# Kernel optimization log

Hardware: AMD Instinct MI355X
Metric: run time of the kernel (lower is better)

## Reference

```python
import jax, jax.numpy as jnp
import numpy as np

B, DIM, SIZE = 16, 512, 128

def _conv2d(x, w, pad_h, pad_w):
    # x: [B,C,H,W], w: [O,I,kh,kw]
    return jax.lax.conv_general_dilated(
        x, w, window_strides=(1, 1),
        padding=((pad_h, pad_h), (pad_w, pad_w)),
        dimension_numbers=('NCHW', 'OIHW', 'NCHW'))


def setup_inputs() -> dict:
    key = jax.random.key(0)
    ks = jax.random.split(key, 8)
    s = SIZE
    return {
        'x': jax.random.normal(ks[0], (B, DIM, s, s), dtype=jnp.float32),
        'w_conv': jax.random.normal(ks[1], (2, DIM, 1, 1), dtype=jnp.float32) * (1.0 / np.sqrt(DIM)),
        'w_ww_conv': jax.random.normal(ks[2], (1, 2, s, 5), dtype=jnp.float32) * (1.0 / np.sqrt(2 * s * 5)),
        'w_hw_conv': jax.random.normal(ks[3], (1, 2, 5, s), dtype=jnp.float32) * (1.0 / np.sqrt(2 * s * 5)),
        'ww_lin_w': jax.random.normal(ks[4], (s, s), dtype=jnp.float32) * (1.0 / np.sqrt(s)),
        'ww_lin_b': jax.random.normal(ks[5], (s,), dtype=jnp.float32) * 0.01,
        'hw_lin_w': jax.random.normal(ks[6], (s, s), dtype=jnp.float32) * (1.0 / np.sqrt(s)),
        'hw_lin_b': jax.random.normal(ks[7], (s,), dtype=jnp.float32) * 0.01,
    }


def reference(x, w_conv, w_ww_conv, w_hw_conv, ww_lin_w, ww_lin_b, hw_lin_w, hw_lin_b):
    # 1x1 conv dim -> 2 (no bias, no bn, no act): pure channel GEMM
    x2 = jnp.einsum('bchw,oc->bohw', x, w_conv[:, :, 0, 0])  # [B,2,S,S]

    # ww branch: conv kernel (SIZE,5), pad (0,2) -> [B,1,1,S]
    ww = _conv2d(x2, w_ww_conv, 0, 2)[:, 0, 0, :]            # [B,S]
    ww = jax.nn.sigmoid(ww @ ww_lin_w.T + ww_lin_b)          # Linear + Sigmoid

    # hw branch: conv kernel (5,SIZE), pad (2,0) -> [B,1,S,1]
    hw = _conv2d(x2, w_hw_conv, 2, 0)[:, 0, :, 0]            # [B,S]
    hw = jax.nn.sigmoid(hw @ hw_lin_w.T + hw_lin_b)

    # batched outer product hw (S,1) @ ww (1,S) -> [B,S,S]
    return jnp.einsum('bh,bw->bhw', hw, ww)
```

## Files before the change

kernel.cpp:

```cpp
#include <hip/hip_runtime.h>
#include <math.h>

#define BB   16
#define CC   512
#define SS   128
#define HWSZ (SS * SS)
#define NCH  16
#define CK   (CC / NCH)

__global__ __launch_bounds__(1024) void k1a_partial(
    const float* __restrict__ x, const float* __restrict__ wconv,
    float* __restrict__ part)
{
    const int b   = blockIdx.x >> 4;
    const int ck  = blockIdx.x & (NCH - 1);
    const int tid = threadIdx.x;

    const float* xp = x + ((size_t)b * CC + (size_t)ck * CK) * HWSZ + tid * 4;
    const float* wA = wconv + ck * CK;
    const float* wB = wconv + CC + ck * CK;

    float4 a0[4], a1[4];
    #pragma unroll
    for (int s = 0; s < 4; ++s) {
        a0[s] = make_float4(0.f, 0.f, 0.f, 0.f);
        a1[s] = make_float4(0.f, 0.f, 0.f, 0.f);
    }

    #pragma unroll 2
    for (int c = 0; c < CK; ++c) {
        const float wa = wA[c];
        const float wb = wB[c];
        #pragma unroll
        for (int s = 0; s < 4; ++s) {
            const float4 v = *(const float4*)(xp + (size_t)c * HWSZ + s * 4096);
            a0[s].x = fmaf(v.x, wa, a0[s].x);
            a0[s].y = fmaf(v.y, wa, a0[s].y);
            a0[s].z = fmaf(v.z, wa, a0[s].z);
            a0[s].w = fmaf(v.w, wa, a0[s].w);
            a1[s].x = fmaf(v.x, wb, a1[s].x);
            a1[s].y = fmaf(v.y, wb, a1[s].y);
            a1[s].z = fmaf(v.z, wb, a1[s].z);
            a1[s].w = fmaf(v.w, wb, a1[s].w);
        }
    }

    float* pp = part + (size_t)(b * NCH + ck) * 2 * HWSZ + tid * 4;
    #pragma unroll
    for (int s = 0; s < 4; ++s) {
        *(float4*)(pp + s * 4096)        = a0[s];
        *(float4*)(pp + HWSZ + s * 4096) = a1[s];
    }
}

__global__ __launch_bounds__(256) void k1b_reduce(
    const float* __restrict__ part, float* __restrict__ x2,
    float* __restrict__ x2t)
{
    const int pc  = blockIdx.x & 15;
    const int o   = (blockIdx.x >> 4) & 1;
    const int b   = blockIdx.x >> 5;
    const int tid = threadIdx.x;

    const int p = (pc * 256 + tid) * 4;

    const float* pp = part + ((size_t)(b * NCH) * 2 + o) * HWSZ + p;
    float4 s = make_float4(0.f, 0.f, 0.f, 0.f);
    #pragma unroll
    for (int ck = 0; ck < NCH; ++ck) {
        const float4 v = *(const float4*)(pp + (size_t)ck * 2 * HWSZ);
        s.x += v.x; s.y += v.y; s.z += v.z; s.w += v.w;
    }

    *(float4*)&x2[(size_t)(b * 2 + o) * HWSZ + p] = s;

    const int h  = p >> 7;
    const int w0 = p & 127;
    float* t = x2t + ((size_t)(b * 2 + o) * SS + w0) * SS + h;
    t[0 * SS] = s.x;
    t[1 * SS] = s.y;
    t[2 * SS] = s.z;
    t[3 * SS] = s.w;
}

__global__ __launch_bounds__(512) void k2_rest(
    const float* __restrict__ x2, const float* __restrict__ x2t,
    const float* __restrict__ wwc,
    const float* __restrict__ hwc,
    const float* __restrict__ wlw, const float* __restrict__ wlb,
    const float* __restrict__ hlw, const float* __restrict__ hlb,
    float* __restrict__ out)
{
    __shared__ float tw[2][5][SS];
    __shared__ float uh[2][5][SS];
    __shared__ float vbuf[2 * SS];
    __shared__ float rbuf[2 * SS];

    const int b        = blockIdx.x;
    const int tid      = threadIdx.x;
    const int lane_pos = tid & 127;
    const int q        = tid >> 7;
    const int half     = q & 1;
    const int half_u   = __builtin_amdgcn_readfirstlane(half);

    if (q < 2) {
        const float* xrow = x2 + (size_t)(b * 2 + half) * HWSZ + lane_pos;
        const float* wrow = wwc + half_u * (SS * 5);
        float acc[5] = {0.f, 0.f, 0.f, 0.f, 0.f};
        #pragma unroll 8
        for (int kh = 0; kh < SS; ++kh) {
            const float xv = xrow[(size_t)kh * SS];
            #pragma unroll
            for (int kw = 0; kw < 5; ++kw)
                acc[kw] = fmaf(xv, wrow[kh * 5 + kw], acc[kw]);
        }
        #pragma unroll
        for (int kw = 0; kw < 5; ++kw) tw[half][kw][lane_pos] = acc[kw];
    } else {
        const float* xcol = x2t + (size_t)(b * 2 + half) * HWSZ + lane_pos;
        const float* wrow = hwc + half_u * (5 * SS);
        float acc[5] = {0.f, 0.f, 0.f, 0.f, 0.f};
        #pragma unroll 8
        for (int kw = 0; kw < SS; ++kw) {
            const float xv = xcol[(size_t)kw * SS];
            #pragma unroll
            for (int kh = 0; kh < 5; ++kh)
                acc[kh] = fmaf(xv, wrow[kh * SS + kw], acc[kh]);
        }
        #pragma unroll
        for (int kh = 0; kh < 5; ++kh) uh[half][kh][lane_pos] = acc[kh];
    }
    __syncthreads();

    if (tid < 256) {
        float s = 0.f;
        if (half == 0) {
            const int wo = lane_pos;
            #pragma unroll
            for (int kw = 0; kw < 5; ++kw) {
                const int wsrc = wo + kw - 2;
                if (wsrc >= 0 && wsrc < SS) s += tw[0][kw][wsrc] + tw[1][kw][wsrc];
            }
        } else {
            const int ho = lane_pos;
            #pragma unroll
            for (int kh = 0; kh < 5; ++kh) {
                const int hsrc = ho + kh - 2;
                if (hsrc >= 0 && hsrc < SS) s += uh[0][kh][hsrc] + uh[1][kh][hsrc];
            }
        }
        vbuf[tid] = s;
    }
    __syncthreads();

    if (tid < 256) {
        const int j = lane_pos;
        const float* lw  = (half == 0) ? wlw : hlw;
        const float* lb  = (half == 0) ? wlb : hlb;
        const float* vin = vbuf + half * SS;
        float s = lb[j];
        const float4* wr = (const float4*)(lw + (size_t)j * SS);
        #pragma unroll 4
        for (int k4 = 0; k4 < SS / 4; ++k4) {
            const float4 wv = wr[k4];
            s = fmaf(vin[4 * k4 + 0], wv.x, s);
            s = fmaf(vin[4 * k4 + 1], wv.y, s);
            s = fmaf(vin[4 * k4 + 2], wv.z, s);
            s = fmaf(vin[4 * k4 + 3], wv.w, s);
        }
        rbuf[tid] = 1.f / (1.f + expf(-s));
    }
    __syncthreads();

    {
        float* ob = out + (size_t)b * HWSZ;
        for (int p4 = tid; p4 < HWSZ / 4; p4 += 512) {
            const int h  = p4 >> 5;
            const int w0 = (p4 & 31) * 4;
            const float hv = rbuf[SS + h];
            float4 o;
            o.x = hv * rbuf[w0 + 0];
            o.y = hv * rbuf[w0 + 1];
            o.z = hv * rbuf[w0 + 2];
            o.w = hv * rbuf[w0 + 3];
            *(float4*)(ob + (size_t)h * SS + w0) = o;
        }
    }
}

extern "C" void kernel_launch(void* const* d_in, const int* in_sizes, int n_in,
                              void* d_out, int out_size, void* d_ws, size_t ws_size,
                              hipStream_t stream) {
    const float* x     = (const float*)d_in[0];
    const float* wconv = (const float*)d_in[1];
    const float* wwc   = (const float*)d_in[2];
    const float* hwc   = (const float*)d_in[3];
    const float* wlw   = (const float*)d_in[4];
    const float* wlb   = (const float*)d_in[5];
    const float* hlw   = (const float*)d_in[6];
    const float* hlb   = (const float*)d_in[7];
    float* out = (float*)d_out;

    float* x2   = (float*)d_ws;
    float* x2t  = x2 + (size_t)BB * 2 * HWSZ;
    float* part = x2t + (size_t)BB * 2 * HWSZ;

    k1a_partial<<<dim3(BB * NCH), dim3(1024), 0, stream>>>(x, wconv, part);
    k1b_reduce<<<dim3(BB * 2 * 16), dim3(256), 0, stream>>>(part, x2, x2t);
    k2_rest<<<dim3(BB), dim3(512), 0, stream>>>(x2, x2t, wwc, hwc,
                                                wlw, wlb, hlw, hlb, out);
}
```

Baseline: 707.9 us.

## Fuse partial-sum reduction into final kernel using LDS tile, drop transposed buffer

Removes the separate reduce kernel and the x2/x2t global buffers. Each batch block now sums the channel partials directly into a padded shared-memory tile and runs both strip convolutions from LDS, splitting the reduction axis across 1024 threads. The first kernel also switches to nontemporal loads with a deeper unroll. The trade-off is that the 32 MB partial reduction now runs on only 16 blocks, and the kernel needs a large LDS allocation.

```diff
diff --git a/kernel.cpp b/kernel.cpp
--- a/kernel.cpp
+++ b/kernel.cpp
@@ -7,6 +7,9 @@
 #define HWSZ (SS * SS)
 #define NCH  16
 #define CK   (CC / NCH)
+#define LP   (SS + 1)
+
+typedef float f4 __attribute__((ext_vector_type(4)));
 
 __global__ __launch_bounds__(1024) void k1a_partial(
     const float* __restrict__ x, const float* __restrict__ wconv,
@@ -20,20 +23,18 @@
     const float* wA = wconv + ck * CK;
     const float* wB = wconv + CC + ck * CK;
 
-    float4 a0[4], a1[4];
+    f4 a0[4], a1[4];
     #pragma unroll
-    for (int s = 0; s < 4; ++s) {
-        a0[s] = make_float4(0.f, 0.f, 0.f, 0.f);
-        a1[s] = make_float4(0.f, 0.f, 0.f, 0.f);
-    }
-
-    #pragma unroll 2
+    for (int s = 0; s < 4; ++s) { a0[s] = (f4)0.f; a1[s] = (f4)0.f; }
+
+    #pragma unroll 4
     for (int c = 0; c < CK; ++c) {
         const float wa = wA[c];
         const float wb = wB[c];
         #pragma unroll
         for (int s = 0; s < 4; ++s) {
-            const float4 v = *(const float4*)(xp + (size_t)c * HWSZ + s * 4096);
+            const f4 v = __builtin_nontemporal_load(
+                (const f4*)(xp + (size_t)c * HWSZ + s * 4096));
             a0[s].x = fmaf(v.x, wa, a0[s].x);
             a0[s].y = fmaf(v.y, wa, a0[s].y);
             a0[s].z = fmaf(v.z, wa, a0[s].z);
@@ -48,105 +49,106 @@
     float* pp = part + (size_t)(b * NCH + ck) * 2 * HWSZ + tid * 4;
     #pragma unroll
     for (int s = 0; s < 4; ++s) {
-        *(float4*)(pp + s * 4096)        = a0[s];
-        *(float4*)(pp + HWSZ + s * 4096) = a1[s];
+        *(f4*)(pp + s * 4096)        = a0[s];
+        *(f4*)(pp + HWSZ + s * 4096) = a1[s];
     }
 }
 
-__global__ __launch_bounds__(256) void k1b_reduce(
-    const float* __restrict__ part, float* __restrict__ x2,
-    float* __restrict__ x2t)
-{
-    const int pc  = blockIdx.x & 15;
-    const int o   = (blockIdx.x >> 4) & 1;
-    const int b   = blockIdx.x >> 5;
-    const int tid = threadIdx.x;
-
-    const int p = (pc * 256 + tid) * 4;
-
-    const float* pp = part + ((size_t)(b * NCH) * 2 + o) * HWSZ + p;
-    float4 s = make_float4(0.f, 0.f, 0.f, 0.f);
-    #pragma unroll
-    for (int ck = 0; ck < NCH; ++ck) {
-        const float4 v = *(const float4*)(pp + (size_t)ck * 2 * HWSZ);
-        s.x += v.x; s.y += v.y; s.z += v.z; s.w += v.w;
-    }
-
-    *(float4*)&x2[(size_t)(b * 2 + o) * HWSZ + p] = s;
-
-    const int h  = p >> 7;
-    const int w0 = p & 127;
-    float* t = x2t + ((size_t)(b * 2 + o) * SS + w0) * SS + h;
-    t[0 * SS] = s.x;
-    t[1 * SS] = s.y;
-    t[2 * SS] = s.z;
-    t[3 * SS] = s.w;
-}
-
-__global__ __launch_bounds__(512) void k2_rest(
-    const float* __restrict__ x2, const float* __restrict__ x2t,
+__global__ __launch_bounds__(1024) void k2_rest(
+    const float* __restrict__ part,
     const float* __restrict__ wwc,
     const float* __restrict__ hwc,
     const float* __restrict__ wlw, const float* __restrict__ wlb,
     const float* __restrict__ hlw, const float* __restrict__ hlb,
     float* __restrict__ out)
 {
-    __shared__ float tw[2][5][SS];
-    __shared__ float uh[2][5][SS];
+    __shared__ float x2l[2][SS][LP];
+    __shared__ float tw2[2][2][5][SS];
+    __shared__ float uh2[2][2][5][SS];
     __shared__ float vbuf[2 * SS];
     __shared__ float rbuf[2 * SS];
 
-    const int b        = blockIdx.x;
-    const int tid      = threadIdx.x;
-    const int lane_pos = tid & 127;
-    const int q        = tid >> 7;
-    const int half     = q & 1;
-    const int half_u   = __builtin_amdgcn_readfirstlane(half);
-
-    if (q < 2) {
-        const float* xrow = x2 + (size_t)(b * 2 + half) * HWSZ + lane_pos;
-        const float* wrow = wwc + half_u * (SS * 5);
+    const int b   = blockIdx.x;
+    const int tid = threadIdx.x;
+
+    {
+        const float* pb = part + (size_t)b * NCH * 2 * HWSZ;
+        #pragma unroll
+        for (int it = 0; it < (2 * HWSZ / 4) / 1024; ++it) {
+            const int q4 = it * 1024 + tid;
+            const int p  = q4 * 4;
+            const float* pp = pb + p;
+            f4 s = (f4)0.f;
+            #pragma unroll
+            for (int c = 0; c < NCH; ++c) {
+                const f4 v = *(const f4*)(pp + (size_t)c * 2 * HWSZ);
+                s.x += v.x; s.y += v.y; s.z += v.z; s.w += v.w;
+            }
+            const int o   = p >> 14;
+            const int pix = p & (HWSZ - 1);
+            const int h   = pix >> 7;
+            const int w   = pix & (SS - 1);
+            x2l[o][h][w + 0] = s.x;
+            x2l[o][h][w + 1] = s.y;
+            x2l[o][h][w + 2] = s.z;
+            x2l[o][h][w + 3] = s.w;
+        }
+    }
+    __syncthreads();
+
+    {
+        const int lane = tid & 127;
+        const int i    = (tid >> 7) & 1;
+        const int br   = (tid >> 8) & 1;
+        const int kp   = tid >> 9;
         float acc[5] = {0.f, 0.f, 0.f, 0.f, 0.f};
-        #pragma unroll 8
-        for (int kh = 0; kh < SS; ++kh) {
-            const float xv = xrow[(size_t)kh * SS];
-            #pragma unroll
-            for (int kw = 0; kw < 5; ++kw)
-                acc[kw] = fmaf(xv, wrow[kh * 5 + kw], acc[kw]);
-        }
-        #pragma unroll
-        for (int kw = 0; kw < 5; ++kw) tw[half][kw][lane_pos] = acc[kw];
-    } else {
-        const float* xcol = x2t + (size_t)(b * 2 + half) * HWSZ + lane_pos;
-        const float* wrow = hwc + half_u * (5 * SS);
-        float acc[5] = {0.f, 0.f, 0.f, 0.f, 0.f};
-        #pragma unroll 8
-        for (int kw = 0; kw < SS; ++kw) {
-            const float xv = xcol[(size_t)kw * SS];
-            #pragma unroll
-            for (int kh = 0; kh < 5; ++kh)
-                acc[kh] = fmaf(xv, wrow[kh * SS + kw], acc[kh]);
-        }
-        #pragma unroll
-        for (int kh = 0; kh < 5; ++kh) uh[half][kh][lane_pos] = acc[kh];
+
+        if (br == 0) {
+            const float* wrow = wwc + i * (SS * 5);
+            const int kh0 = kp * 64;
+            #pragma unroll 8
+            for (int kh = kh0; kh < kh0 + 64; ++kh) {
+                const float xv = x2l[i][kh][lane];
+                #pragma unroll
+                for (int kw = 0; kw < 5; ++kw)
+                    acc[kw] = fmaf(xv, wrow[kh * 5 + kw], acc[kw]);
+            }
+            #pragma unroll
+            for (int kw = 0; kw < 5; ++kw) tw2[kp][i][kw][lane] = acc[kw];
+        } else {
+            const float* wrow = hwc + i * (5 * SS);
+            const int kw0 = kp * 64;
+            #pragma unroll 8
+            for (int kw = kw0; kw < kw0 + 64; ++kw) {
+                const float xv = x2l[i][lane][kw];
+                #pragma unroll
+                for (int kh = 0; kh < 5; ++kh)
+                    acc[kh] = fmaf(xv, wrow[kh * SS + kw], acc[kh]);
+            }
+            #pragma unroll
+            for (int kh = 0; kh < 5; ++kh) uh2[kp][i][kh][lane] = acc[kh];
+        }
     }
     __syncthreads();
 
     if (tid < 256) {
+        const int pos = tid & 127;
         float s = 0.f;
-        if (half == 0) {
-            const int wo = lane_pos;
+        if (tid < 128) {
             #pragma unroll
             for (int kw = 0; kw < 5; ++kw) {
-                const int wsrc = wo + kw - 2;
-                if (wsrc >= 0 && wsrc < SS) s += tw[0][kw][wsrc] + tw[1][kw][wsrc];
+                const int wsrc = pos + kw - 2;
+                if (wsrc >= 0 && wsrc < SS)
+                    s += (tw2[0][0][kw][wsrc] + tw2[0][1][kw][wsrc])
+                       + (tw2[1][0][kw][wsrc] + tw2[1][1][kw][wsrc]);
             }
         } else {
-            const int ho = lane_pos;
             #pragma unroll
             for (int kh = 0; kh < 5; ++kh) {
-                const int hsrc = ho + kh - 2;
-                if (hsrc >= 0 && hsrc < SS) s += uh[0][kh][hsrc] + uh[1][kh][hsrc];
+                const int hsrc = pos + kh - 2;
+                if (hsrc >= 0 && hsrc < SS)
+                    s += (uh2[0][0][kh][hsrc] + uh2[0][1][kh][hsrc])
+                       + (uh2[1][0][kh][hsrc] + uh2[1][1][kh][hsrc]);
             }
         }
         vbuf[tid] = s;
@@ -154,15 +156,16 @@
     __syncthreads();
 
     if (tid < 256) {
-        const int j = lane_pos;
+        const int j    = tid & 127;
+        const int half = tid >> 7;
         const float* lw  = (half == 0) ? wlw : hlw;
         const float* lb  = (half == 0) ? wlb : hlb;
         const float* vin = vbuf + half * SS;
         float s = lb[j];
-        const float4* wr = (const float4*)(lw + (size_t)j * SS);
+        const f4* wr = (const f4*)(lw + (size_t)j * SS);
         #pragma unroll 4
         for (int k4 = 0; k4 < SS / 4; ++k4) {
-            const float4 wv = wr[k4];
+            const f4 wv = wr[k4];
             s = fmaf(vin[4 * k4 + 0], wv.x, s);
             s = fmaf(vin[4 * k4 + 1], wv.y, s);
             s = fmaf(vin[4 * k4 + 2], wv.z, s);
@@ -174,16 +177,18 @@
 
     {
         float* ob = out + (size_t)b * HWSZ;
-        for (int p4 = tid; p4 < HWSZ / 4; p4 += 512) {
+        #pragma unroll
+        for (int it = 0; it < (HWSZ / 4) / 1024; ++it) {
+            const int p4 = it * 1024 + tid;
             const int h  = p4 >> 5;
             const int w0 = (p4 & 31) * 4;
             const float hv = rbuf[SS + h];
-            float4 o;
+            f4 o;
             o.x = hv * rbuf[w0 + 0];
             o.y = hv * rbuf[w0 + 1];
             o.z = hv * rbuf[w0 + 2];
             o.w = hv * rbuf[w0 + 3];
-            *(float4*)(ob + (size_t)h * SS + w0) = o;
+            *(f4*)(ob + (size_t)h * SS + w0) = o;
         }
     }
 }
@@ -201,12 +206,9 @@
     const float* hlb   = (const float*)d_in[7];
     float* out = (float*)d_out;
 
-    float* x2   = (float*)d_ws;
-    float* x2t  = x2 + (size_t)BB * 2 * HWSZ;
-    float* part = x2t + (size_t)BB * 2 * HWSZ;
+    float* part = (float*)d_ws;
 
     k1a_partial<<<dim3(BB * NCH), dim3(1024), 0, stream>>>(x, wconv, part);
-    k1b_reduce<<<dim3(BB * 2 * 16), dim3(256), 0, stream>>>(part, x2, x2t);
-    k2_rest<<<dim3(BB), dim3(512), 0, stream>>>(x2, x2t, wwc, hwc,
-                                                wlw, wlb, hlw, hlb, out);
+    k2_rest<<<dim3(BB), dim3(1024), 0, stream>>>(part, wwc, hwc,
+                                                 wlw, wlb, hlw, hlb, out);
 }
```

New measurement: 689.0 us. 2.7% less time.
